# Kernel optimization log

Hardware: AMD Instinct MI355X
Metric: run time of the kernel (lower is better)

Reference implementation:

```python
import jax, jax.numpy as jnp
import numpy as np

# ---- dims ----
B, NP_, NL = 32, 350, 30          # graphs, protein atoms, ligand atoms per graph
NG = NP_ + NL
N = B * NG                        # 12160 nodes
E = B * NP_ * NL                  # 336000 edges (dense bipartite per graph)
HID, HEADS, G = 128, 16, 20
DH = HID // HEADS
KV = 2 * HID + G                  # 276
R_MIN, R_MAX = 0.0, 10.0


def _mlp_params(key, din, dout, hid=HID):
    k1, k2 = jax.random.split(key)
    return (jax.random.normal(k1, (din, hid), jnp.float32) / np.sqrt(din),
            jnp.zeros((hid,), jnp.float32),
            jnp.ones((hid,), jnp.float32),
            jnp.zeros((hid,), jnp.float32),
            jax.random.normal(k2, (hid, dout), jnp.float32) / np.sqrt(hid),
            jnp.zeros((dout,), jnp.float32))


def setup_inputs() -> dict:
    key = jax.random.key(0)
    h = jax.random.normal(jax.random.fold_in(key, 0), (N, HID), jnp.float32)
    x = jax.random.normal(jax.random.fold_in(key, 1), (N, 3), jnp.float32) * 3.0
    # node layout per graph: NP_ protein atoms then NL ligand atoms
    mask_ligand = np.tile(np.concatenate([np.zeros(NP_, np.int64), np.ones(NL, np.int64)]), B)
    base = (np.arange(B) * NG)[:, None]
    prot = base + np.arange(NP_)[None, :]            # [B, NP_]
    lig = base + NP_ + np.arange(NL)[None, :]        # [B, NL]
    # torch: dst = repeat_interleave(protein, NL); src = ligand.repeat(NP_)
    dst = np.repeat(prot, NL, axis=1).reshape(-1)
    src = np.tile(lig, (1, NP_)).reshape(-1)
    inp = {"h": h, "x": x, "src": jnp.asarray(src), "dst": jnp.asarray(dst),
           "mask_ligand": jnp.asarray(mask_ligand)}
    dims = {"hk": (KV, HID), "hv": (KV, HID), "xv": (KV, HEADS), "hq": (HID, HID), "no": (2 * HID, HID)}
    for i, (nm, (di, do)) in enumerate(dims.items()):
        for s, arr in zip(("w1", "b1", "g", "be", "w2", "b2"), _mlp_params(jax.random.fold_in(key, 10 + i), di, do)):
            inp[f"{nm}_{s}"] = arr
    return inp


def _mlp(t, w1, b1, g, be, w2, b2):
    # Linear -> LayerNorm -> ReLU -> Linear
    y = t @ w1 + b1
    mu = y.mean(-1, keepdims=True)
    var = ((y - mu) ** 2).mean(-1, keepdims=True)
    y = jax.nn.relu((y - mu) * jax.lax.rsqrt(var + 1e-5) * g + be)
    return y @ w2 + b2


def _forward(h, x, src, dst, mask_ligand, ps):
    rel_x = x[src] - x[dst]                                   # [E,3]
    dist = jnp.linalg.norm(rel_x, axis=-1, keepdims=True)     # [E,1]
    offset = jnp.linspace(R_MIN, R_MAX, G)
    coeff = -0.5 / (offset[1] - offset[0]) ** 2
    r_feat = jnp.exp(coeff * (dist - offset) ** 2)            # [E,G]; outer_product(v) == v
    # inner layer unpacks (dst_i, src_i) = (src, dst): hi=h[src_i]=h[dst], hj=h[dst_i]=h[src]
    kv = jnp.concatenate([r_feat, h[dst], h[src]], -1)        # [E,KV]
    k = _mlp(kv, *ps["hk"]).reshape(-1, HEADS, DH)            # [E,H,dh]
    q = _mlp(h, *ps["hq"]).reshape(-1, HEADS, DH)             # [N,H,dh]
    logits = (q[src] * k).sum(-1) / np.sqrt(DH)               # [E,H]
    # scatter_softmax over dst_i = src groups (ligand nodes)
    smax = jax.ops.segment_max(logits, src, num_segments=N)
    ex = jnp.exp(logits - smax[src])
    alpha = ex / jax.ops.segment_sum(ex, src, num_segments=N)[src]   # [E,H]
    v = _mlp(kv, *ps["hv"]).reshape(-1, HEADS, DH)            # [E,H,dh]
    xv = _mlp(kv, *ps["xv"])                                  # [E,H]
    m = alpha[:, :, None] * v                                 # [E,H,dh]
    mx = (alpha * xv)[:, :, None] * rel_x[:, None, :]         # [E,H,3]
    out = jax.ops.segment_sum(m, src, num_segments=N).reshape(N, HID)
    out_x = jax.ops.segment_sum(mx, src, num_segments=N)      # [N,H,3]
    # out_fc: h_in[mask_ligand] with int64 mask gathers rows 0/1 (faithful to source)
    out = _mlp(jnp.concatenate([out, h[mask_ligand]], -1), *ps["no"])
    h_out = out + h
    x_out = x + out_x.mean(1)
    return h_out, x_out


def reference(h, x, src, dst, mask_ligand,
              hk_w1, hk_b1, hk_g, hk_be, hk_w2, hk_b2,
              hv_w1, hv_b1, hv_g, hv_be, hv_w2, hv_b2,
              xv_w1, xv_b1, xv_g, xv_be, xv_w2, xv_b2,
              hq_w1, hq_b1, hq_g, hq_be, hq_w2, hq_b2,
              no_w1, no_b1, no_g, no_be, no_w2, no_b2):
    ps = {"hk": (hk_w1, hk_b1, hk_g, hk_be, hk_w2, hk_b2),
          "hv": (hv_w1, hv_b1, hv_g, hv_be, hv_w2, hv_b2),
          "xv": (xv_w1, xv_b1, xv_g, xv_be, xv_w2, xv_b2),
          "hq": (hq_w1, hq_b1, hq_g, hq_be, hq_w2, hq_b2),
          "no": (no_w1, no_b1, no_g, no_be, no_w2, no_b2)}
    return _forward(h, x, src, dst, mask_ligand, ps)
```

## Files before the change

### kernel.cpp

```cpp
#include <hip/hip_runtime.h>
#include <math.h>

namespace {
constexpr int kB = 32;
constexpr int kNP = 350;
constexpr int kNL = 30;
constexpr int kNG = 380;
constexpr int kN = kB * kNG;
constexpr int kG = 20;
constexpr int kNPROT = kB * kNP;
constexpr int kNLIG = kB * kNL;
constexpr int TP = 32;
constexpr int NT = 11;
}

__global__ __launch_bounds__(256) void pre_kernel(
    const float* __restrict__ h,
    const float* __restrict__ wk1, const float* __restrict__ bk1,
    const float* __restrict__ wv1, const float* __restrict__ bv1,
    const float* __restrict__ wx1, const float* __restrict__ bx1,
    float* __restrict__ outKd, float* __restrict__ outVd, float* __restrict__ outXd,
    float* __restrict__ outKs, float* __restrict__ outVs, float* __restrict__ outXs) {
  const int m = blockIdx.y;
  const float* w1 = (m == 0) ? wk1 : (m == 1) ? wv1 : wx1;
  const float* b1 = (m == 0) ? bk1 : (m == 1) ? bv1 : bx1;
  const bool isProt = (blockIdx.x < 175);
  const int rbase = isProt ? blockIdx.x * 64 : (blockIdx.x - 175) * 64;
  float* outArr = isProt ? ((m == 0) ? outKd : (m == 1) ? outVd : outXd)
                         : ((m == 0) ? outKs : (m == 1) ? outVs : outXs);
  const float* wb = w1 + (isProt ? 20 * 128 : 148 * 128);

  __shared__ float sh[64 * 132];
  const int t = threadIdx.x;
#pragma unroll
  for (int j = 0; j < 8; ++j) {
    int flat = t + j * 256;
    int row = flat >> 5;
    int col = (flat & 31) * 4;
    int r = rbase + row;
    int node;
    if (isProt) node = (r / kNP) * kNG + (r % kNP);
    else        node = (r / kNL) * kNG + kNP + (r % kNL);
    *(float4*)&sh[row * 132 + col] = *(const float4*)(h + (size_t)node * 128 + col);
  }
  __syncthreads();

  const int dcol = (t & 31) * 4;
  const int rrow = (t >> 5) * 8;
  float4 acc[8];
#pragma unroll
  for (int i = 0; i < 8; ++i) acc[i] = make_float4(0.f, 0.f, 0.f, 0.f);

  for (int k = 0; k < 128; k += 4) {
    float4 a4[8];
#pragma unroll
    for (int i = 0; i < 8; ++i) a4[i] = *(float4*)&sh[(rrow + i) * 132 + k];
#pragma unroll
    for (int kk = 0; kk < 4; ++kk) {
      float4 w4 = *(const float4*)(wb + (size_t)(k + kk) * 128 + dcol);
#pragma unroll
      for (int i = 0; i < 8; ++i) {
        float a = (kk == 0) ? a4[i].x : (kk == 1) ? a4[i].y : (kk == 2) ? a4[i].z : a4[i].w;
        acc[i].x += a * w4.x; acc[i].y += a * w4.y;
        acc[i].z += a * w4.z; acc[i].w += a * w4.w;
      }
    }
  }
  float4 bias = make_float4(0.f, 0.f, 0.f, 0.f);
  if (!isProt) bias = *(const float4*)(b1 + dcol);
#pragma unroll
  for (int i = 0; i < 8; ++i) {
    float4 o = acc[i];
    o.x += bias.x; o.y += bias.y; o.z += bias.z; o.w += bias.w;
    *(float4*)(outArr + (size_t)(rbase + rrow + i) * 128 + dcol) = o;
  }
}

__global__ __launch_bounds__(128) void cvec_kernel(
    const float* __restrict__ h,
    const float* __restrict__ no_w1, const float* __restrict__ no_b1,
    const float* __restrict__ no_g, const float* __restrict__ no_be,
    const float* __restrict__ no_w2, const float* __restrict__ no_b2,
    float* __restrict__ cvec) {
  __shared__ float sy[128];
  __shared__ float sa[128];
  __shared__ float red[2];
  const int d = threadIdx.x;
  float y = no_b1[d];
  for (int i = 0; i < 128; ++i) y += h[i] * no_w1[(size_t)(128 + i) * 128 + d];
  sy[d] = y;
  __syncthreads();
  if (d == 0) {
    float s = 0.f, ss = 0.f;
    for (int i = 0; i < 128; ++i) { s += sy[i]; ss += sy[i] * sy[i]; }
    float mu = s / 128.f;
    red[0] = mu;
    red[1] = rsqrtf(ss / 128.f - mu * mu + 1e-5f);
  }
  __syncthreads();
  float a = (y - red[0]) * red[1] * no_g[d] + no_be[d];
  sa[d] = fmaxf(a, 0.f);
  __syncthreads();
  float o = no_b2[d];
  for (int i = 0; i < 128; ++i) o += sa[i] * no_w2[(size_t)i * 128 + d];
  cvec[d] = o;
}

__global__ __launch_bounds__(256) void prot_kernel(
    const float* __restrict__ h, const float* __restrict__ x,
    const float* __restrict__ cvec, float* __restrict__ hout, float* __restrict__ xout) {
  int idx = blockIdx.x * 256 + threadIdx.x;
  if (idx < kNPROT * 32) {
    int r = idx >> 5, c4 = (idx & 31) * 4;
    int node = (r / kNP) * kNG + (r % kNP);
    float4 hv = *(const float4*)(h + (size_t)node * 128 + c4);
    float4 cv = *(const float4*)(cvec + c4);
    *(float4*)(hout + (size_t)node * 128 + c4) =
        make_float4(hv.x + cv.x, hv.y + cv.y, hv.z + cv.z, hv.w + cv.w);
  }
  if (idx < kNPROT * 3) {
    int r = idx / 3, c = idx % 3;
    int node = (r / kNP) * kNG + (r % kNP);
    xout[(size_t)node * 3 + c] = x[(size_t)node * 3 + c];
  }
}

struct W20 {
  float4 a0, a1, a2, a3, a4, a5, a6, a7, a8, a9;
  float4 a10, a11, a12, a13, a14, a15, a16, a17, a18, a19;
};

__device__ __forceinline__ W20 load_w20(const float* __restrict__ W, int c4) {
  W20 r;
  r.a0  = *(const float4*)(W + 0 * 128 + c4);
  r.a1  = *(const float4*)(W + 1 * 128 + c4);
  r.a2  = *(const float4*)(W + 2 * 128 + c4);
  r.a3  = *(const float4*)(W + 3 * 128 + c4);
  r.a4  = *(const float4*)(W + 4 * 128 + c4);
  r.a5  = *(const float4*)(W + 5 * 128 + c4);
  r.a6  = *(const float4*)(W + 6 * 128 + c4);
  r.a7  = *(const float4*)(W + 7 * 128 + c4);
  r.a8  = *(const float4*)(W + 8 * 128 + c4);
  r.a9  = *(const float4*)(W + 9 * 128 + c4);
  r.a10 = *(const float4*)(W + 10 * 128 + c4);
  r.a11 = *(const float4*)(W + 11 * 128 + c4);
  r.a12 = *(const float4*)(W + 12 * 128 + c4);
  r.a13 = *(const float4*)(W + 13 * 128 + c4);
  r.a14 = *(const float4*)(W + 14 * 128 + c4);
  r.a15 = *(const float4*)(W + 15 * 128 + c4);
  r.a16 = *(const float4*)(W + 16 * 128 + c4);
  r.a17 = *(const float4*)(W + 17 * 128 + c4);
  r.a18 = *(const float4*)(W + 18 * 128 + c4);
  r.a19 = *(const float4*)(W + 19 * 128 + c4);
  return r;
}

__device__ __forceinline__ float4 gemm20(const W20& w, const float* rfp, float4 yv) {
  const float4 ra = *(const float4*)(rfp + 0);
  const float4 rb = *(const float4*)(rfp + 4);
  const float4 rc = *(const float4*)(rfp + 8);
  const float4 rd = *(const float4*)(rfp + 12);
  const float4 re = *(const float4*)(rfp + 16);
  yv.x += ra.x * w.a0.x;  yv.y += ra.x * w.a0.y;  yv.z += ra.x * w.a0.z;  yv.w += ra.x * w.a0.w;
  yv.x += ra.y * w.a1.x;  yv.y += ra.y * w.a1.y;  yv.z += ra.y * w.a1.z;  yv.w += ra.y * w.a1.w;
  yv.x += ra.z * w.a2.x;  yv.y += ra.z * w.a2.y;  yv.z += ra.z * w.a2.z;  yv.w += ra.z * w.a2.w;
  yv.x += ra.w * w.a3.x;  yv.y += ra.w * w.a3.y;  yv.z += ra.w * w.a3.z;  yv.w += ra.w * w.a3.w;
  yv.x += rb.x * w.a4.x;  yv.y += rb.x * w.a4.y;  yv.z += rb.x * w.a4.z;  yv.w += rb.x * w.a4.w;
  yv.x += rb.y * w.a5.x;  yv.y += rb.y * w.a5.y;  yv.z += rb.y * w.a5.z;  yv.w += rb.y * w.a5.w;
  yv.x += rb.z * w.a6.x;  yv.y += rb.z * w.a6.y;  yv.z += rb.z * w.a6.z;  yv.w += rb.z * w.a6.w;
  yv.x += rb.w * w.a7.x;  yv.y += rb.w * w.a7.y;  yv.z += rb.w * w.a7.z;  yv.w += rb.w * w.a7.w;
  yv.x += rc.x * w.a8.x;  yv.y += rc.x * w.a8.y;  yv.z += rc.x * w.a8.z;  yv.w += rc.x * w.a8.w;
  yv.x += rc.y * w.a9.x;  yv.y += rc.y * w.a9.y;  yv.z += rc.y * w.a9.z;  yv.w += rc.y * w.a9.w;
  yv.x += rc.z * w.a10.x; yv.y += rc.z * w.a10.y; yv.z += rc.z * w.a10.z; yv.w += rc.z * w.a10.w;
  yv.x += rc.w * w.a11.x; yv.y += rc.w * w.a11.y; yv.z += rc.w * w.a11.z; yv.w += rc.w * w.a11.w;
  yv.x += rd.x * w.a12.x; yv.y += rd.x * w.a12.y; yv.z += rd.x * w.a12.z; yv.w += rd.x * w.a12.w;
  yv.x += rd.y * w.a13.x; yv.y += rd.y * w.a13.y; yv.z += rd.y * w.a13.z; yv.w += rd.y * w.a13.w;
  yv.x += rd.z * w.a14.x; yv.y += rd.z * w.a14.y; yv.z += rd.z * w.a14.z; yv.w += rd.z * w.a14.w;
  yv.x += rd.w * w.a15.x; yv.y += rd.w * w.a15.y; yv.z += rd.w * w.a15.z; yv.w += rd.w * w.a15.w;
  yv.x += re.x * w.a16.x; yv.y += re.x * w.a16.y; yv.z += re.x * w.a16.z; yv.w += re.x * w.a16.w;
  yv.x += re.y * w.a17.x; yv.y += re.y * w.a17.y; yv.z += re.y * w.a17.z; yv.w += re.y * w.a17.w;
  yv.x += re.z * w.a18.x; yv.y += re.z * w.a18.y; yv.z += re.z * w.a18.z; yv.w += re.z * w.a18.w;
  yv.x += re.w * w.a19.x; yv.y += re.w * w.a19.y; yv.z += re.w * w.a19.z; yv.w += re.w * w.a19.w;
  return yv;
}

__device__ __forceinline__ void ln_relu_store(float4 yv, float4 g4, float4 be4, float* dst) {
  float s = yv.x + yv.y + yv.z + yv.w;
  float ss = yv.x * yv.x + yv.y * yv.y + yv.z * yv.z + yv.w * yv.w;
  for (int m = 16; m; m >>= 1) { s += __shfl_xor(s, m); ss += __shfl_xor(ss, m); }
  float mu = s * (1.f / 128.f);
  float rs = rsqrtf(ss * (1.f / 128.f) - mu * mu + 1e-5f);
  float4 a;
  a.x = fmaxf((yv.x - mu) * rs * g4.x + be4.x, 0.f);
  a.y = fmaxf((yv.y - mu) * rs * g4.y + be4.y, 0.f);
  a.z = fmaxf((yv.z - mu) * rs * g4.z + be4.z, 0.f);
  a.w = fmaxf((yv.w - mu) * rs * g4.w + be4.w, 0.f);
  *(float4*)dst = a;
}

__device__ __forceinline__ float4 addf4(float4 a, float4 b) {
  return make_float4(a.x + b.x, a.y + b.y, a.z + b.z, a.w + b.w);
}

__global__ __launch_bounds__(256, 2) void edge_kernel(
    const float* __restrict__ h, const float* __restrict__ x,
    const float* __restrict__ preKd, const float* __restrict__ preVd, const float* __restrict__ preXd,
    const float* __restrict__ preKs, const float* __restrict__ preVs, const float* __restrict__ preXs,
    const float* __restrict__ hk_w1, const float* __restrict__ hk_g, const float* __restrict__ hk_be,
    const float* __restrict__ hk_w2, const float* __restrict__ hk_b2,
    const float* __restrict__ hv_w1, const float* __restrict__ hv_g, const float* __restrict__ hv_be,
    const float* __restrict__ hv_w2, const float* __restrict__ hv_b2,
    const float* __restrict__ xv_w1, const float* __restrict__ xv_g, const float* __restrict__ xv_be,
    const float* __restrict__ xv_w2, const float* __restrict__ xv_b2,
    const float* __restrict__ hq_w1, const float* __restrict__ hq_b1, const float* __restrict__ hq_g,
    const float* __restrict__ hq_be, const float* __restrict__ hq_w2, const float* __restrict__ hq_b2,
    const float* __restrict__ no_w1, const float* __restrict__ no_b1, const float* __restrict__ no_g,
    const float* __restrict__ no_be, const float* __restrict__ no_w2, const float* __restrict__ no_b2,
    float* __restrict__ hout, float* __restrict__ xout) {

  __shared__ float smem[13236];
  float* const s_qw    = smem;
  float* const s_logit = smem + 2112;
  float* const s_a     = smem + 7712;
  float* const s_rfu   = smem + 11936;
  float* const s_q     = s_rfu;
  float* const s_outv  = s_rfu + 128;
  float* const s_outx  = s_rfu + 256;
  float* const s_dist  = smem + 12576;
  float* const s_tmp   = smem + 12928;
  float* const s_qb    = smem + 13184;
  float* const s_mx    = smem + 13200;
  float* const s_sum   = smem + 13216;
  float* const s_red   = smem + 13232;

  const int wg = blockIdx.x;
  const int g = wg / kNL, l = wg % kNL;
  const int lignode = g * kNG + kNP + l;
  const int ligidx = g * kNL + l;
  const int t = threadIdx.x;
  const int c4 = (t & 31) * 4;
  const int myp = t >> 5;

  constexpr float kStep = 10.f / 19.f;
  constexpr float kCoeff = -0.5f / (kStep * kStep);

  const float lx0 = x[(size_t)lignode * 3 + 0];
  const float lx1 = x[(size_t)lignode * 3 + 1];
  const float lx2 = x[(size_t)lignode * 3 + 2];

  if (t < 32) *(float4*)&s_tmp[t * 4] = *(const float4*)(h + (size_t)lignode * 128 + t * 4);
  for (int p = t; p < kNP; p += 256) {
    const float* xp = x + (size_t)(g * kNG + p) * 3;
    float r0 = lx0 - xp[0], r1 = lx1 - xp[1], r2 = lx2 - xp[2];
    s_dist[p] = sqrtf(r0 * r0 + r1 * r1 + r2 * r2);
  }
  __syncthreads();

  float yq = 0.f;
  if (t < 128) {
    yq = hq_b1[t];
    for (int k = 0; k < 128; ++k) yq += s_tmp[k] * hq_w1[(size_t)k * 128 + t];
    s_a[t] = yq;
  }
  __syncthreads();
  if (t < 64) {
    float v0 = s_a[t], v1 = s_a[t + 64];
    float s = v0 + v1, ss = v0 * v0 + v1 * v1;
#pragma unroll
    for (int off = 32; off; off >>= 1) { s += __shfl_xor(s, off); ss += __shfl_xor(ss, off); }
    if (t == 0) {
      float mu = s / 128.f;
      s_red[0] = mu;
      s_red[1] = rsqrtf(ss / 128.f - mu * mu + 1e-5f);
    }
  }
  __syncthreads();
  if (t < 128) {
    float a = (yq - s_red[0]) * s_red[1] * hq_g[t] + hq_be[t];
    s_tmp[t] = fmaxf(a, 0.f);
  }
  __syncthreads();
  if (t < 128) {
    float qv = hq_b2[t];
    for (int d = 0; d < 128; ++d) qv += s_tmp[d] * hq_w2[(size_t)d * 128 + t];
    s_q[t] = qv;
  }
  __syncthreads();

  constexpr float kInvSqrtDH = 0.35355339059327379f;
#pragma unroll
  for (int i = 0; i < 8; ++i) {
    int idx = t + i * 256;
    int hh = idx >> 7, d = idx & 127;
    float4 wa = *(const float4*)(hk_w2 + (size_t)d * 128 + hh * 8);
    float4 wb = *(const float4*)(hk_w2 + (size_t)d * 128 + hh * 8 + 4);
    float v = wa.x * s_q[hh * 8 + 0] + wa.y * s_q[hh * 8 + 1] + wa.z * s_q[hh * 8 + 2] +
              wa.w * s_q[hh * 8 + 3] + wb.x * s_q[hh * 8 + 4] + wb.y * s_q[hh * 8 + 5] +
              wb.z * s_q[hh * 8 + 6] + wb.w * s_q[hh * 8 + 7];
    s_qw[hh * 132 + d] = v * kInvSqrtDH;
  }
  if (t < 16) {
    float v = 0.f;
#pragma unroll
    for (int j = 0; j < 8; ++j) v += hk_b2[t * 8 + j] * s_q[t * 8 + j];
    s_qb[t] = v * kInvSqrtDH;
  }
  for (int o = t; o < TP * 20; o += 256) {
    int p = o / 20;
    float dd = s_dist[p] - (o - p * 20) * kStep;
    s_rfu[o] = __expf(kCoeff * dd * dd);
  }
  __syncthreads();

  {
    const W20 w = load_w20(hk_w1, c4);
    const float4 g4 = *(const float4*)(hk_g + c4);
    const float4 be4 = *(const float4*)(hk_be + c4);
    const float4 pres4 = *(const float4*)(preKs + (size_t)ligidx * 128 + c4);

    for (int tile = 0; tile < NT; ++tile) {
      const int p0 = tile * TP;
      const int np = (350 - p0) < TP ? (350 - p0) : TP;
      const int i0 = myp, i1 = myp + 8, i2 = myp + 16, i3 = myp + 24;
      float4 pr0, pr1, pr2, pr3;
      const float* base = preKd + (size_t)(g * kNP + p0) * 128 + c4;
      pr0 = *(const float4*)(base + (size_t)i0 * 128);
      pr1 = *(const float4*)(base + (size_t)i1 * 128);
      pr2 = *(const float4*)(base + (size_t)i2 * 128);
      if (i3 < np) pr3 = *(const float4*)(base + (size_t)i3 * 128);
      ln_relu_store(gemm20(w, &s_rfu[i0 * 20], addf4(pres4, pr0)), g4, be4, &s_a[i0 * 132 + c4]);
      ln_relu_store(gemm20(w, &s_rfu[i1 * 20], addf4(pres4, pr1)), g4, be4, &s_a[i1 * 132 + c4]);
      ln_relu_store(gemm20(w, &s_rfu[i2 * 20], addf4(pres4, pr2)), g4, be4, &s_a[i2 * 132 + c4]);
      if (i3 < np)
        ln_relu_store(gemm20(w, &s_rfu[i3 * 20], addf4(pres4, pr3)), g4, be4, &s_a[i3 * 132 + c4]);
      __syncthreads();
      {
        const int p = t & 31;
        const int h0 = (t >> 5) * 2, h1 = h0 + 1;
        float f0 = 0.f, f1 = 0.f;
#pragma unroll
        for (int d = 0; d < 128; d += 4) {
          float4 a4 = *(float4*)&s_a[p * 132 + d];
          float4 q0 = *(float4*)&s_qw[h0 * 132 + d];
          float4 q1 = *(float4*)&s_qw[h1 * 132 + d];
          f0 += a4.x * q0.x + a4.y * q0.y + a4.z * q0.z + a4.w * q0.w;
          f1 += a4.x * q1.x + a4.y * q1.y + a4.z * q1.z + a4.w * q1.w;
        }
        if (p < np) {
          s_logit[(p0 + p) * 16 + h0] = f0 + s_qb[h0];
          s_logit[(p0 + p) * 16 + h1] = f1 + s_qb[h1];
        }
        const int nxt = (tile + 1 == NT) ? 0 : tile + 1;
        const int q0p = nxt * TP;
        const int nq = (350 - q0p) < TP ? (350 - q0p) : TP;
        for (int o = t; o < nq * 20; o += 256) {
          int pp = o / 20;
          float dd = s_dist[q0p + pp] - (o - pp * 20) * kStep;
          s_rfu[o] = __expf(kCoeff * dd * dd);
        }
      }
      __syncthreads();
    }
  }

  {
    int hh = t & 15, ck = t >> 4;
    float mx = -1e30f;
    for (int p = ck; p < 350; p += 16) mx = fmaxf(mx, s_logit[p * 16 + hh]);
    s_tmp[t] = mx;
  }
  __syncthreads();
  if (t < 16) {
    float mx = s_tmp[t];
    for (int c = 1; c < 16; ++c) mx = fmaxf(mx, s_tmp[c * 16 + t]);
    s_mx[t] = mx;
  }
  __syncthreads();
  {
    int hh = t & 15, ck = t >> 4;
    float mx = s_mx[hh], sm = 0.f;
    for (int p = ck; p < 350; p += 16) sm += __expf(s_logit[p * 16 + hh] - mx);
    s_tmp[t] = sm;
  }
  __syncthreads();
  if (t < 16) {
    float sm = 0.f;
    for (int c = 0; c < 16; ++c) sm += s_tmp[c * 16 + t];
    s_sum[t] = 1.f / sm;
  }
  __syncthreads();
  for (int o = t; o < 350 * 16; o += 256) {
    int hh = o & 15;
    s_logit[o] = __expf(s_logit[o] - s_mx[hh]) * s_sum[hh];
  }
  for (int o = t; o < 2048; o += 256) {
    int hh = o >> 7, d = o & 127;
    s_qw[hh * 132 + d] = xv_w2[(size_t)d * 16 + hh];
  }
  if (t < 16) s_qb[t] = xv_b2[t];
  __syncthreads();

  float accv0 = 0.f, accv1 = 0.f, accv2 = 0.f, accv3 = 0.f;
  float accv4 = 0.f, accv5 = 0.f, accv6 = 0.f, accv7 = 0.f;
  const int dd_ = t & 127;
  const int hb8 = (t >> 7) * 8;
  {
    const W20 w = load_w20(hv_w1, c4);
    const float4 g4 = *(const float4*)(hv_g + c4);
    const float4 be4 = *(const float4*)(hv_be + c4);
    const float4 pres4 = *(const float4*)(preVs + (size_t)ligidx * 128 + c4);

    for (int tile = 0; tile < NT; ++tile) {
      const int p0 = tile * TP;
      const int np = (350 - p0) < TP ? (350 - p0) : TP;
      const int i0 = myp, i1 = myp + 8, i2 = myp + 16, i3 = myp + 24;
      float4 pr0, pr1, pr2, pr3;
      const float* base = preVd + (size_t)(g * kNP + p0) * 128 + c4;
      pr0 = *(const float4*)(base + (size_t)i0 * 128);
      pr1 = *(const float4*)(base + (size_t)i1 * 128);
      pr2 = *(const float4*)(base + (size_t)i2 * 128);
      if (i3 < np) pr3 = *(const float4*)(base + (size_t)i3 * 128);
      ln_relu_store(gemm20(w, &s_rfu[i0 * 20], addf4(pres4, pr0)), g4, be4, &s_a[i0 * 132 + c4]);
      ln_relu_store(gemm20(w, &s_rfu[i1 * 20], addf4(pres4, pr1)), g4, be4, &s_a[i1 * 132 + c4]);
      ln_relu_store(gemm20(w, &s_rfu[i2 * 20], addf4(pres4, pr2)), g4, be4, &s_a[i2 * 132 + c4]);
      if (i3 < np)
        ln_relu_store(gemm20(w, &s_rfu[i3 * 20], addf4(pres4, pr3)), g4, be4, &s_a[i3 * 132 + c4]);
      __syncthreads();
      for (int p = 0; p < np; ++p) {
        float av = s_a[p * 132 + dd_];
        float4 alA = *(float4*)&s_logit[(p0 + p) * 16 + hb8];
        float4 alB = *(float4*)&s_logit[(p0 + p) * 16 + hb8 + 4];
        accv0 += alA.x * av; accv1 += alA.y * av;
        accv2 += alA.z * av; accv3 += alA.w * av;
        accv4 += alB.x * av; accv5 += alB.y * av;
        accv6 += alB.z * av; accv7 += alB.w * av;
      }
      {
        const int nxt = (tile + 1 == NT) ? 0 : tile + 1;
        const int q0p = nxt * TP;
        const int nq = (350 - q0p) < TP ? (350 - q0p) : TP;
        for (int o = t; o < nq * 20; o += 256) {
          int pp = o / 20;
          float dd2 = s_dist[q0p + pp] - (o - pp * 20) * kStep;
          s_rfu[o] = __expf(kCoeff * dd2 * dd2);
        }
      }
      __syncthreads();
    }
  }

  float ax0 = 0.f, ax1 = 0.f, ax2 = 0.f, ax3 = 0.f, ax4 = 0.f, ax5 = 0.f;
  {
    const W20 w = load_w20(xv_w1, c4);
    const float4 g4 = *(const float4*)(xv_g + c4);
    const float4 be4 = *(const float4*)(xv_be + c4);
    const float4 pres4 = *(const float4*)(preXs + (size_t)ligidx * 128 + c4);
    const int p_ = t & 31;
    const int h0 = (t >> 5) * 2, h1 = h0 + 1;

    for (int tile = 0; tile < NT; ++tile) {
      const int p0 = tile * TP;
      const int np = (350 - p0) < TP ? (350 - p0) : TP;
      const int i0 = myp, i1 = myp + 8, i2 = myp + 16, i3 = myp + 24;
      float4 pr0, pr1, pr2, pr3;
      const float* base = preXd + (size_t)(g * kNP + p0) * 128 + c4;
      pr0 = *(const float4*)(base + (size_t)i0 * 128);
      pr1 = *(const float4*)(base + (size_t)i1 * 128);
      pr2 = *(const float4*)(base + (size_t)i2 * 128);
      if (i3 < np) pr3 = *(const float4*)(base + (size_t)i3 * 128);
      ln_relu_store(gemm20(w, &s_rfu[i0 * 20], addf4(pres4, pr0)), g4, be4, &s_a[i0 * 132 + c4]);
      ln_relu_store(gemm20(w, &s_rfu[i1 * 20], addf4(pres4, pr1)), g4, be4, &s_a[i1 * 132 + c4]);
      ln_relu_store(gemm20(w, &s_rfu[i2 * 20], addf4(pres4, pr2)), g4, be4, &s_a[i2 * 132 + c4]);
      if (i3 < np)
        ln_relu_store(gemm20(w, &s_rfu[i3 * 20], addf4(pres4, pr3)), g4, be4, &s_a[i3 * 132 + c4]);
      __syncthreads();
      {
        float f0 = 0.f, f1 = 0.f;
#pragma unroll
        for (int d = 0; d < 128; d += 4) {
          float4 a4 = *(float4*)&s_a[p_ * 132 + d];
          float4 q0 = *(float4*)&s_qw[h0 * 132 + d];
          float4 q1 = *(float4*)&s_qw[h1 * 132 + d];
          f0 += a4.x * q0.x + a4.y * q0.y + a4.z * q0.z + a4.w * q0.w;
          f1 += a4.x * q1.x + a4.y * q1.y + a4.z * q1.z + a4.w * q1.w;
        }
        float w0 = 0.f, w1 = 0.f, r0 = 0.f, r1 = 0.f, r2 = 0.f;
        if (p_ < np) {
          int pg = p0 + p_;
          w0 = s_logit[pg * 16 + h0] * (f0 + s_qb[h0]);
          w1 = s_logit[pg * 16 + h1] * (f1 + s_qb[h1]);
          const float* xp = x + (size_t)(g * kNG + pg) * 3;
          r0 = lx0 - xp[0]; r1 = lx1 - xp[1]; r2 = lx2 - xp[2];
        }
        float p00 = w0 * r0, p01 = w0 * r1, p02 = w0 * r2;
        float p10 = w1 * r0, p11 = w1 * r1, p12 = w1 * r2;
#pragma unroll
        for (int m = 16; m; m >>= 1) {
          p00 += __shfl_xor(p00, m); p01 += __shfl_xor(p01, m); p02 += __shfl_xor(p02, m);
          p10 += __shfl_xor(p10, m); p11 += __shfl_xor(p11, m); p12 += __shfl_xor(p12, m);
        }
        ax0 += p00; ax1 += p01; ax2 += p02;
        ax3 += p10; ax4 += p11; ax5 += p12;
      }
      {
        const int nxt = (tile + 1 == NT) ? 0 : tile + 1;
        const int q0p = nxt * TP;
        const int nq = (350 - q0p) < TP ? (350 - q0p) : TP;
        for (int o = t; o < nq * 20; o += 256) {
          int pp = o / 20;
          float dd2 = s_dist[q0p + pp] - (o - pp * 20) * kStep;
          s_rfu[o] = __expf(kCoeff * dd2 * dd2);
        }
      }
      __syncthreads();
    }
  }

  s_a[(hb8 + 0) * 132 + dd_] = accv0;
  s_a[(hb8 + 1) * 132 + dd_] = accv1;
  s_a[(hb8 + 2) * 132 + dd_] = accv2;
  s_a[(hb8 + 3) * 132 + dd_] = accv3;
  s_a[(hb8 + 4) * 132 + dd_] = accv4;
  s_a[(hb8 + 5) * 132 + dd_] = accv5;
  s_a[(hb8 + 6) * 132 + dd_] = accv6;
  s_a[(hb8 + 7) * 132 + dd_] = accv7;
  {
    const int h0 = (t >> 5) * 2;
    if ((t & 31) == 0) {
      s_outx[h0 * 4 + 0] = ax0; s_outx[h0 * 4 + 1] = ax1; s_outx[h0 * 4 + 2] = ax2;
      s_outx[(h0 + 1) * 4 + 0] = ax3; s_outx[(h0 + 1) * 4 + 1] = ax4;
      s_outx[(h0 + 1) * 4 + 2] = ax5;
    }
  }
  __syncthreads();

  if (t < 128) {
    float o = hv_b2[t];
    const int hh = t >> 3;
    for (int d = 0; d < 128; ++d) o += s_a[hh * 132 + d] * hv_w2[(size_t)d * 128 + t];
    s_outv[t] = o;
  }
  if (t >= 128 && t < 131) {
    int c = t - 128;
    float sm = 0.f;
#pragma unroll
    for (int hh = 0; hh < 16; ++hh) sm += s_outx[hh * 4 + c];
    xout[(size_t)lignode * 3 + c] = x[(size_t)lignode * 3 + c] + sm * (1.f / 16.f);
  }
  __syncthreads();
  float yn = 0.f;
  if (t < 128) {
    yn = no_b1[t];
    for (int i = 0; i < 128; ++i) yn += s_outv[i] * no_w1[(size_t)i * 128 + t];
    const float* h1 = h + 128;
    for (int i = 0; i < 128; ++i) yn += h1[i] * no_w1[(size_t)(128 + i) * 128 + t];
    s_tmp[t] = yn;
  }
  __syncthreads();
  if (t < 64) {
    float v0 = s_tmp[t], v1 = s_tmp[t + 64];
    float s = v0 + v1, ss = v0 * v0 + v1 * v1;
#pragma unroll
    for (int off = 32; off; off >>= 1) { s += __shfl_xor(s, off); ss += __shfl_xor(ss, off); }
    if (t == 0) {
      float mu = s / 128.f;
      s_red[0] = mu;
      s_red[1] = rsqrtf(ss / 128.f - mu * mu + 1e-5f);
    }
  }
  __syncthreads();
  if (t < 128) {
    float a = (yn - s_red[0]) * s_red[1] * no_g[t] + no_be[t];
    s_outv[t] = fmaxf(a, 0.f);
  }
  __syncthreads();
  if (t < 128) {
    float o = no_b2[t];
    for (int d = 0; d < 128; ++d) o += s_outv[d] * no_w2[(size_t)d * 128 + t];
    hout[(size_t)lignode * 128 + t] = o + h[(size_t)lignode * 128 + t];
  }
}

extern "C" void kernel_launch(void* const* d_in, const int* in_sizes, int n_in,
                              void* d_out, int out_size, void* d_ws, size_t ws_size,
                              hipStream_t stream) {
  (void)in_sizes; (void)n_in; (void)out_size; (void)ws_size;
  const float* h = (const float*)d_in[0];
  const float* x = (const float*)d_in[1];
  const float* hk_w1 = (const float*)d_in[5];
  const float* hk_b1 = (const float*)d_in[6];
  const float* hk_g  = (const float*)d_in[7];
  const float* hk_be = (const float*)d_in[8];
  const float* hk_w2 = (const float*)d_in[9];
  const float* hk_b2 = (const float*)d_in[10];
  const float* hv_w1 = (const float*)d_in[11];
  const float* hv_b1 = (const float*)d_in[12];
  const float* hv_g  = (const float*)d_in[13];
  const float* hv_be = (const float*)d_in[14];
  const float* hv_w2 = (const float*)d_in[15];
  const float* hv_b2 = (const float*)d_in[16];
  const float* xv_w1 = (const float*)d_in[17];
  const float* xv_b1 = (const float*)d_in[18];
  const float* xv_g  = (const float*)d_in[19];
  const float* xv_be = (const float*)d_in[20];
  const float* xv_w2 = (const float*)d_in[21];
  const float* xv_b2 = (const float*)d_in[22];
  const float* hq_w1 = (const float*)d_in[23];
  const float* hq_b1 = (const float*)d_in[24];
  const float* hq_g  = (const float*)d_in[25];
  const float* hq_be = (const float*)d_in[26];
  const float* hq_w2 = (const float*)d_in[27];
  const float* hq_b2 = (const float*)d_in[28];
  const float* no_w1 = (const float*)d_in[29];
  const float* no_b1 = (const float*)d_in[30];
  const float* no_g  = (const float*)d_in[31];
  const float* no_be = (const float*)d_in[32];
  const float* no_w2 = (const float*)d_in[33];
  const float* no_b2 = (const float*)d_in[34];

  float* ws = (float*)d_ws;
  float* preKd = ws;
  float* preVd = preKd + (size_t)kNPROT * 128;
  float* preXd = preVd + (size_t)kNPROT * 128;
  float* preKs = preXd + (size_t)kNPROT * 128;
  float* preVs = preKs + (size_t)kNLIG * 128;
  float* preXs = preVs + (size_t)kNLIG * 128;
  float* cvec  = preXs + (size_t)kNLIG * 128;

  float* hout = (float*)d_out;
  float* xout = hout + (size_t)kN * 128;

  pre_kernel<<<dim3(190, 3), dim3(256), 0, stream>>>(
      h, hk_w1, hk_b1, hv_w1, hv_b1, xv_w1, xv_b1,
      preKd, preVd, preXd, preKs, preVs, preXs);
  cvec_kernel<<<dim3(1), dim3(128), 0, stream>>>(
      h, no_w1, no_b1, no_g, no_be, no_w2, no_b2, cvec);
  edge_kernel<<<dim3(960), dim3(256), 0, stream>>>(
      h, x, preKd, preVd, preXd, preKs, preVs, preXs,
      hk_w1, hk_g, hk_be, hk_w2, hk_b2,
      hv_w1, hv_g, hv_be, hv_w2, hv_b2,
      xv_w1, xv_g, xv_be, xv_w2, xv_b2,
      hq_w1, hq_b1, hq_g, hq_be, hq_w2, hq_b2,
      no_w1, no_b1, no_g, no_be, no_w2, no_b2,
      hout, xout);
  prot_kernel<<<dim3(1400), dim3(256), 0, stream>>>(h, x, cvec, hout, xout);
}
```

Before: 694.7 us.

## Restructure edge first-layer GEMM to stream weights and block contiguous rows per thread

The per-thread register-resident 20x4 weight block (W20) is replaced by a loop that loads each weight row from global memory once per tile and applies it to four contiguous protein rows. The RBF features are stored transposed (gaussian-major, padded stride 36) so one float4 shared load feeds four rows. This cuts register pressure, which is why the launch bound drops its minimum-blocks-per-CU hint. The q-weight stride also changes from 132 to 128. The cost is repeated global/L1 weight loads inside the tile loop and possible LDS bank conflicts from the unpadded 128 stride.

```diff
diff --git a/kernel.cpp b/kernel.cpp
--- a/kernel.cpp
+++ b/kernel.cpp
@@ -125,68 +125,10 @@
   }
 }
 
-struct W20 {
-  float4 a0, a1, a2, a3, a4, a5, a6, a7, a8, a9;
-  float4 a10, a11, a12, a13, a14, a15, a16, a17, a18, a19;
-};
-
-__device__ __forceinline__ W20 load_w20(const float* __restrict__ W, int c4) {
-  W20 r;
-  r.a0  = *(const float4*)(W + 0 * 128 + c4);
-  r.a1  = *(const float4*)(W + 1 * 128 + c4);
-  r.a2  = *(const float4*)(W + 2 * 128 + c4);
-  r.a3  = *(const float4*)(W + 3 * 128 + c4);
-  r.a4  = *(const float4*)(W + 4 * 128 + c4);
-  r.a5  = *(const float4*)(W + 5 * 128 + c4);
-  r.a6  = *(const float4*)(W + 6 * 128 + c4);
-  r.a7  = *(const float4*)(W + 7 * 128 + c4);
-  r.a8  = *(const float4*)(W + 8 * 128 + c4);
-  r.a9  = *(const float4*)(W + 9 * 128 + c4);
-  r.a10 = *(const float4*)(W + 10 * 128 + c4);
-  r.a11 = *(const float4*)(W + 11 * 128 + c4);
-  r.a12 = *(const float4*)(W + 12 * 128 + c4);
-  r.a13 = *(const float4*)(W + 13 * 128 + c4);
-  r.a14 = *(const float4*)(W + 14 * 128 + c4);
-  r.a15 = *(const float4*)(W + 15 * 128 + c4);
-  r.a16 = *(const float4*)(W + 16 * 128 + c4);
-  r.a17 = *(const float4*)(W + 17 * 128 + c4);
-  r.a18 = *(const float4*)(W + 18 * 128 + c4);
-  r.a19 = *(const float4*)(W + 19 * 128 + c4);
-  return r;
-}
-
-__device__ __forceinline__ float4 gemm20(const W20& w, const float* rfp, float4 yv) {
-  const float4 ra = *(const float4*)(rfp + 0);
-  const float4 rb = *(const float4*)(rfp + 4);
-  const float4 rc = *(const float4*)(rfp + 8);
-  const float4 rd = *(const float4*)(rfp + 12);
-  const float4 re = *(const float4*)(rfp + 16);
-  yv.x += ra.x * w.a0.x;  yv.y += ra.x * w.a0.y;  yv.z += ra.x * w.a0.z;  yv.w += ra.x * w.a0.w;
-  yv.x += ra.y * w.a1.x;  yv.y += ra.y * w.a1.y;  yv.z += ra.y * w.a1.z;  yv.w += ra.y * w.a1.w;
-  yv.x += ra.z * w.a2.x;  yv.y += ra.z * w.a2.y;  yv.z += ra.z * w.a2.z;  yv.w += ra.z * w.a2.w;
-  yv.x += ra.w * w.a3.x;  yv.y += ra.w * w.a3.y;  yv.z += ra.w * w.a3.z;  yv.w += ra.w * w.a3.w;
-  yv.x += rb.x * w.a4.x;  yv.y += rb.x * w.a4.y;  yv.z += rb.x * w.a4.z;  yv.w += rb.x * w.a4.w;
-  yv.x += rb.y * w.a5.x;  yv.y += rb.y * w.a5.y;  yv.z += rb.y * w.a5.z;  yv.w += rb.y * w.a5.w;
-  yv.x += rb.z * w.a6.x;  yv.y += rb.z * w.a6.y;  yv.z += rb.z * w.a6.z;  yv.w += rb.z * w.a6.w;
-  yv.x += rb.w * w.a7.x;  yv.y += rb.w * w.a7.y;  yv.z += rb.w * w.a7.z;  yv.w += rb.w * w.a7.w;
-  yv.x += rc.x * w.a8.x;  yv.y += rc.x * w.a8.y;  yv.z += rc.x * w.a8.z;  yv.w += rc.x * w.a8.w;
-  yv.x += rc.y * w.a9.x;  yv.y += rc.y * w.a9.y;  yv.z += rc.y * w.a9.z;  yv.w += rc.y * w.a9.w;
-  yv.x += rc.z * w.a10.x; yv.y += rc.z * w.a10.y; yv.z += rc.z * w.a10.z; yv.w += rc.z * w.a10.w;
-  yv.x += rc.w * w.a11.x; yv.y += rc.w * w.a11.y; yv.z += rc.w * w.a11.z; yv.w += rc.w * w.a11.w;
-  yv.x += rd.x * w.a12.x; yv.y += rd.x * w.a12.y; yv.z += rd.x * w.a12.z; yv.w += rd.x * w.a12.w;
-  yv.x += rd.y * w.a13.x; yv.y += rd.y * w.a13.y; yv.z += rd.y * w.a13.z; yv.w += rd.y * w.a13.w;
-  yv.x += rd.z * w.a14.x; yv.y += rd.z * w.a14.y; yv.z += rd.z * w.a14.z; yv.w += rd.z * w.a14.w;
-  yv.x += rd.w * w.a15.x; yv.y += rd.w * w.a15.y; yv.z += rd.w * w.a15.z; yv.w += rd.w * w.a15.w;
-  yv.x += re.x * w.a16.x; yv.y += re.x * w.a16.y; yv.z += re.x * w.a16.z; yv.w += re.x * w.a16.w;
-  yv.x += re.y * w.a17.x; yv.y += re.y * w.a17.y; yv.z += re.y * w.a17.z; yv.w += re.y * w.a17.w;
-  yv.x += re.z * w.a18.x; yv.y += re.z * w.a18.y; yv.z += re.z * w.a18.z; yv.w += re.z * w.a18.w;
-  yv.x += re.w * w.a19.x; yv.y += re.w * w.a19.y; yv.z += re.w * w.a19.z; yv.w += re.w * w.a19.w;
-  return yv;
-}
-
-__device__ __forceinline__ void ln_relu_store(float4 yv, float4 g4, float4 be4, float* dst) {
+__device__ __forceinline__ void ln_row_store(float4 yv, float4 g4, float4 be4, float* dst) {
   float s = yv.x + yv.y + yv.z + yv.w;
   float ss = yv.x * yv.x + yv.y * yv.y + yv.z * yv.z + yv.w * yv.w;
+#pragma unroll
   for (int m = 16; m; m >>= 1) { s += __shfl_xor(s, m); ss += __shfl_xor(ss, m); }
   float mu = s * (1.f / 128.f);
   float rs = rsqrtf(ss * (1.f / 128.f) - mu * mu + 1e-5f);
@@ -198,11 +140,11 @@
   *(float4*)dst = a;
 }
 
-__device__ __forceinline__ float4 addf4(float4 a, float4 b) {
-  return make_float4(a.x + b.x, a.y + b.y, a.z + b.z, a.w + b.w);
-}
-
-__global__ __launch_bounds__(256, 2) void edge_kernel(
+__device__ __forceinline__ void fma4(float4& a, float s, float4 w) {
+  a.x += s * w.x; a.y += s * w.y; a.z += s * w.z; a.w += s * w.w;
+}
+
+__global__ __launch_bounds__(256) void edge_kernel(
     const float* __restrict__ h, const float* __restrict__ x,
     const float* __restrict__ preKd, const float* __restrict__ preVd, const float* __restrict__ preXd,
     const float* __restrict__ preKs, const float* __restrict__ preVs, const float* __restrict__ preXs,
@@ -218,20 +160,20 @@
     const float* __restrict__ no_be, const float* __restrict__ no_w2, const float* __restrict__ no_b2,
     float* __restrict__ hout, float* __restrict__ xout) {
 
-  __shared__ float smem[13236];
+  __shared__ float smem[13250];
   float* const s_qw    = smem;
-  float* const s_logit = smem + 2112;
-  float* const s_a     = smem + 7712;
-  float* const s_rfu   = smem + 11936;
-  float* const s_q     = s_rfu;
-  float* const s_outv  = s_rfu + 128;
-  float* const s_outx  = s_rfu + 256;
-  float* const s_dist  = smem + 12576;
-  float* const s_tmp   = smem + 12928;
-  float* const s_qb    = smem + 13184;
-  float* const s_mx    = smem + 13200;
-  float* const s_sum   = smem + 13216;
-  float* const s_red   = smem + 13232;
+  float* const s_logit = smem + 2048;
+  float* const s_a     = smem + 7648;
+  float* const s_rft   = smem + 11872;
+  float* const s_q     = s_rft;
+  float* const s_outv  = s_rft + 128;
+  float* const s_outx  = s_rft + 256;
+  float* const s_dist  = smem + 12592;
+  float* const s_tmp   = smem + 12944;
+  float* const s_qb    = smem + 13200;
+  float* const s_mx    = smem + 13216;
+  float* const s_sum   = smem + 13232;
+  float* const s_red   = smem + 13248;
 
   const int wg = blockIdx.x;
   const int g = wg / kNL, l = wg % kNL;
@@ -297,7 +239,7 @@
     float v = wa.x * s_q[hh * 8 + 0] + wa.y * s_q[hh * 8 + 1] + wa.z * s_q[hh * 8 + 2] +
               wa.w * s_q[hh * 8 + 3] + wb.x * s_q[hh * 8 + 4] + wb.y * s_q[hh * 8 + 5] +
               wb.z * s_q[hh * 8 + 6] + wb.w * s_q[hh * 8 + 7];
-    s_qw[hh * 132 + d] = v * kInvSqrtDH;
+    s_qw[hh * 128 + d] = v * kInvSqrtDH;
   }
   if (t < 16) {
     float v = 0.f;
@@ -305,15 +247,15 @@
     for (int j = 0; j < 8; ++j) v += hk_b2[t * 8 + j] * s_q[t * 8 + j];
     s_qb[t] = v * kInvSqrtDH;
   }
+  __syncthreads();
   for (int o = t; o < TP * 20; o += 256) {
-    int p = o / 20;
-    float dd = s_dist[p] - (o - p * 20) * kStep;
-    s_rfu[o] = __expf(kCoeff * dd * dd);
+    int p = o & 31, gg = o >> 5;
+    float dd = s_dist[p] - gg * kStep;
+    s_rft[gg * 36 + p] = __expf(kCoeff * dd * dd);
   }
   __syncthreads();
 
   {
-    const W20 w = load_w20(hk_w1, c4);
     const float4 g4 = *(const float4*)(hk_g + c4);
     const float4 be4 = *(const float4*)(hk_be + c4);
     const float4 pres4 = *(const float4*)(preKs + (size_t)ligidx * 128 + c4);
@@ -321,18 +263,28 @@
     for (int tile = 0; tile < NT; ++tile) {
       const int p0 = tile * TP;
       const int np = (350 - p0) < TP ? (350 - p0) : TP;
-      const int i0 = myp, i1 = myp + 8, i2 = myp + 16, i3 = myp + 24;
-      float4 pr0, pr1, pr2, pr3;
+      const int r0 = myp * 4;
       const float* base = preKd + (size_t)(g * kNP + p0) * 128 + c4;
-      pr0 = *(const float4*)(base + (size_t)i0 * 128);
-      pr1 = *(const float4*)(base + (size_t)i1 * 128);
-      pr2 = *(const float4*)(base + (size_t)i2 * 128);
-      if (i3 < np) pr3 = *(const float4*)(base + (size_t)i3 * 128);
-      ln_relu_store(gemm20(w, &s_rfu[i0 * 20], addf4(pres4, pr0)), g4, be4, &s_a[i0 * 132 + c4]);
-      ln_relu_store(gemm20(w, &s_rfu[i1 * 20], addf4(pres4, pr1)), g4, be4, &s_a[i1 * 132 + c4]);
-      ln_relu_store(gemm20(w, &s_rfu[i2 * 20], addf4(pres4, pr2)), g4, be4, &s_a[i2 * 132 + c4]);
-      if (i3 < np)
-        ln_relu_store(gemm20(w, &s_rfu[i3 * 20], addf4(pres4, pr3)), g4, be4, &s_a[i3 * 132 + c4]);
+      float4 a0 = make_float4(0.f, 0.f, 0.f, 0.f), a1 = a0, a2 = a0, a3 = a0;
+      if (r0 + 0 < np) { float4 v = *(const float4*)(base + (size_t)(r0 + 0) * 128);
+        a0 = make_float4(pres4.x + v.x, pres4.y + v.y, pres4.z + v.z, pres4.w + v.w); }
+      if (r0 + 1 < np) { float4 v = *(const float4*)(base + (size_t)(r0 + 1) * 128);
+        a1 = make_float4(pres4.x + v.x, pres4.y + v.y, pres4.z + v.z, pres4.w + v.w); }
+      if (r0 + 2 < np) { float4 v = *(const float4*)(base + (size_t)(r0 + 2) * 128);
+        a2 = make_float4(pres4.x + v.x, pres4.y + v.y, pres4.z + v.z, pres4.w + v.w); }
+      if (r0 + 3 < np) { float4 v = *(const float4*)(base + (size_t)(r0 + 3) * 128);
+        a3 = make_float4(pres4.x + v.x, pres4.y + v.y, pres4.z + v.z, pres4.w + v.w); }
+#pragma unroll 4
+      for (int gg = 0; gg < 20; ++gg) {
+        const float4 w4 = *(const float4*)(hk_w1 + gg * 128 + c4);
+        const float4 rf4 = *(const float4*)&s_rft[gg * 36 + r0];
+        fma4(a0, rf4.x, w4); fma4(a1, rf4.y, w4);
+        fma4(a2, rf4.z, w4); fma4(a3, rf4.w, w4);
+      }
+      if (r0 + 0 < np) ln_row_store(a0, g4, be4, &s_a[(r0 + 0) * 132 + c4]);
+      if (r0 + 1 < np) ln_row_store(a1, g4, be4, &s_a[(r0 + 1) * 132 + c4]);
+      if (r0 + 2 < np) ln_row_store(a2, g4, be4, &s_a[(r0 + 2) * 132 + c4]);
+      if (r0 + 3 < np) ln_row_store(a3, g4, be4, &s_a[(r0 + 3) * 132 + c4]);
       __syncthreads();
       {
         const int p = t & 31;
@@ -341,8 +293,8 @@
 #pragma unroll
         for (int d = 0; d < 128; d += 4) {
           float4 a4 = *(float4*)&s_a[p * 132 + d];
-          float4 q0 = *(float4*)&s_qw[h0 * 132 + d];
-          float4 q1 = *(float4*)&s_qw[h1 * 132 + d];
+          float4 q0 = *(float4*)&s_qw[h0 * 128 + d];
+          float4 q1 = *(float4*)&s_qw[h1 * 128 + d];
           f0 += a4.x * q0.x + a4.y * q0.y + a4.z * q0.z + a4.w * q0.w;
           f1 += a4.x * q1.x + a4.y * q1.y + a4.z * q1.z + a4.w * q1.w;
         }
@@ -353,10 +305,11 @@
         const int nxt = (tile + 1 == NT) ? 0 : tile + 1;
         const int q0p = nxt * TP;
         const int nq = (350 - q0p) < TP ? (350 - q0p) : TP;
-        for (int o = t; o < nq * 20; o += 256) {
-          int pp = o / 20;
-          float dd = s_dist[q0p + pp] - (o - pp * 20) * kStep;
-          s_rfu[o] = __expf(kCoeff * dd * dd);
+        for (int o = t; o < 640; o += 256) {
+          int pp = o & 31, gg = o >> 5;
+          float v = 0.f;
+          if (pp < nq) { float dd = s_dist[q0p + pp] - gg * kStep; v = __expf(kCoeff * dd * dd); }
+          s_rft[gg * 36 + pp] = v;
         }
       }
       __syncthreads();
@@ -395,7 +348,7 @@
   }
   for (int o = t; o < 2048; o += 256) {
     int hh = o >> 7, d = o & 127;
-    s_qw[hh * 132 + d] = xv_w2[(size_t)d * 16 + hh];
+    s_qw[hh * 128 + d] = xv_w2[(size_t)d * 16 + hh];
   }
   if (t < 16) s_qb[t] = xv_b2[t];
   __syncthreads();
@@ -405,7 +358,6 @@
   const int dd_ = t & 127;
   const int hb8 = (t >> 7) * 8;
   {
-    const W20 w = load_w20(hv_w1, c4);
     const float4 g4 = *(const float4*)(hv_g + c4);
     const float4 be4 = *(const float4*)(hv_be + c4);
     const float4 pres4 = *(const float4*)(preVs + (size_t)ligidx * 128 + c4);
@@ -413,18 +365,28 @@
     for (int tile = 0; tile < NT; ++tile) {
       const int p0 = tile * TP;
       const int np = (350 - p0) < TP ? (350 - p0) : TP;
-      const int i0 = myp, i1 = myp + 8, i2 = myp + 16, i3 = myp + 24;
-      float4 pr0, pr1, pr2, pr3;
+      const int r0 = myp * 4;
       const float* base = preVd + (size_t)(g * kNP + p0) * 128 + c4;
-      pr0 = *(const float4*)(base + (size_t)i0 * 128);
-      pr1 = *(const float4*)(base + (size_t)i1 * 128);
-      pr2 = *(const float4*)(base + (size_t)i2 * 128);
-      if (i3 < np) pr3 = *(const float4*)(base + (size_t)i3 * 128);
-      ln_relu_store(gemm20(w, &s_rfu[i0 * 20], addf4(pres4, pr0)), g4, be4, &s_a[i0 * 132 + c4]);
-      ln_relu_store(gemm20(w, &s_rfu[i1 * 20], addf4(pres4, pr1)), g4, be4, &s_a[i1 * 132 + c4]);
-      ln_relu_store(gemm20(w, &s_rfu[i2 * 20], addf4(pres4, pr2)), g4, be4, &s_a[i2 * 132 + c4]);
-      if (i3 < np)
-        ln_relu_store(gemm20(w, &s_rfu[i3 * 20], addf4(pres4, pr3)), g4, be4, &s_a[i3 * 132 + c4]);
+      float4 a0 = make_float4(0.f, 0.f, 0.f, 0.f), a1 = a0, a2 = a0, a3 = a0;
+      if (r0 + 0 < np) { float4 v = *(const float4*)(base + (size_t)(r0 + 0) * 128);
+        a0 = make_float4(pres4.x + v.x, pres4.y + v.y, pres4.z + v.z, pres4.w + v.w); }
+      if (r0 + 1 < np) { float4 v = *(const float4*)(base + (size_t)(r0 + 1) * 128);
+        a1 = make_float4(pres4.x + v.x, pres4.y + v.y, pres4.z + v.z, pres4.w + v.w); }
+      if (r0 + 2 < np) { float4 v = *(const float4*)(base + (size_t)(r0 + 2) * 128);
+        a2 = make_float4(pres4.x + v.x, pres4.y + v.y, pres4.z + v.z, pres4.w + v.w); }
+      if (r0 + 3 < np) { float4 v = *(const float4*)(base + (size_t)(r0 + 3) * 128);
+        a3 = make_float4(pres4.x + v.x, pres4.y + v.y, pres4.z + v.z, pres4.w + v.w); }
+#pragma unroll 4
+      for (int gg = 0; gg < 20; ++gg) {
+        const float4 w4 = *(const float4*)(hv_w1 + gg * 128 + c4);
+        const float4 rf4 = *(const float4*)&s_rft[gg * 36 + r0];
+        fma4(a0, rf4.x, w4); fma4(a1, rf4.y, w4);
+        fma4(a2, rf4.z, w4); fma4(a3, rf4.w, w4);
+      }
+      if (r0 + 0 < np) ln_row_store(a0, g4, be4, &s_a[(r0 + 0) * 132 + c4]);
+      if (r0 + 1 < np) ln_row_store(a1, g4, be4, &s_a[(r0 + 1) * 132 + c4]);
+      if (r0 + 2 < np) ln_row_store(a2, g4, be4, &s_a[(r0 + 2) * 132 + c4]);
+      if (r0 + 3 < np) ln_row_store(a3, g4, be4, &s_a[(r0 + 3) * 132 + c4]);
       __syncthreads();
       for (int p = 0; p < np; ++p) {
         float av = s_a[p * 132 + dd_];
@@ -439,10 +401,11 @@
         const int nxt = (tile + 1 == NT) ? 0 : tile + 1;
         const int q0p = nxt * TP;
         const int nq = (350 - q0p) < TP ? (350 - q0p) : TP;
-        for (int o = t; o < nq * 20; o += 256) {
-          int pp = o / 20;
-          float dd2 = s_dist[q0p + pp] - (o - pp * 20) * kStep;
-          s_rfu[o] = __expf(kCoeff * dd2 * dd2);
+        for (int o = t; o < 640; o += 256) {
+          int pp = o & 31, gg = o >> 5;
+          float v = 0.f;
+          if (pp < nq) { float dd = s_dist[q0p + pp] - gg * kStep; v = __expf(kCoeff * dd * dd); }
+          s_rft[gg * 36 + pp] = v;
         }
       }
       __syncthreads();
@@ -451,7 +414,6 @@
 
   float ax0 = 0.f, ax1 = 0.f, ax2 = 0.f, ax3 = 0.f, ax4 = 0.f, ax5 = 0.f;
   {
-    const W20 w = load_w20(xv_w1, c4);
     const float4 g4 = *(const float4*)(xv_g + c4);
     const float4 be4 = *(const float4*)(xv_be + c4);
     const float4 pres4 = *(const float4*)(preXs + (size_t)ligidx * 128 + c4);
@@ -461,39 +423,49 @@
     for (int tile = 0; tile < NT; ++tile) {
       const int p0 = tile * TP;
       const int np = (350 - p0) < TP ? (350 - p0) : TP;
-      const int i0 = myp, i1 = myp + 8, i2 = myp + 16, i3 = myp + 24;
-      float4 pr0, pr1, pr2, pr3;
+      const int r0 = myp * 4;
       const float* base = preXd + (size_t)(g * kNP + p0) * 128 + c4;
-      pr0 = *(const float4*)(base + (size_t)i0 * 128);
-      pr1 = *(const float4*)(base + (size_t)i1 * 128);
-      pr2 = *(const float4*)(base + (size_t)i2 * 128);
-      if (i3 < np) pr3 = *(const float4*)(base + (size_t)i3 * 128);
-      ln_relu_store(gemm20(w, &s_rfu[i0 * 20], addf4(pres4, pr0)), g4, be4, &s_a[i0 * 132 + c4]);
-      ln_relu_store(gemm20(w, &s_rfu[i1 * 20], addf4(pres4, pr1)), g4, be4, &s_a[i1 * 132 + c4]);
-      ln_relu_store(gemm20(w, &s_rfu[i2 * 20], addf4(pres4, pr2)), g4, be4, &s_a[i2 * 132 + c4]);
-      if (i3 < np)
-        ln_relu_store(gemm20(w, &s_rfu[i3 * 20], addf4(pres4, pr3)), g4, be4, &s_a[i3 * 132 + c4]);
+      float4 a0 = make_float4(0.f, 0.f, 0.f, 0.f), a1 = a0, a2 = a0, a3 = a0;
+      if (r0 + 0 < np) { float4 v = *(const float4*)(base + (size_t)(r0 + 0) * 128);
+        a0 = make_float4(pres4.x + v.x, pres4.y + v.y, pres4.z + v.z, pres4.w + v.w); }
+      if (r0 + 1 < np) { float4 v = *(const float4*)(base + (size_t)(r0 + 1) * 128);
+        a1 = make_float4(pres4.x + v.x, pres4.y + v.y, pres4.z + v.z, pres4.w + v.w); }
+      if (r0 + 2 < np) { float4 v = *(const float4*)(base + (size_t)(r0 + 2) * 128);
+        a2 = make_float4(pres4.x + v.x, pres4.y + v.y, pres4.z + v.z, pres4.w + v.w); }
+      if (r0 + 3 < np) { float4 v = *(const float4*)(base + (size_t)(r0 + 3) * 128);
+        a3 = make_float4(pres4.x + v.x, pres4.y + v.y, pres4.z + v.z, pres4.w + v.w); }
+#pragma unroll 4
+      for (int gg = 0; gg < 20; ++gg) {
+        const float4 w4 = *(const float4*)(xv_w1 + gg * 128 + c4);
+        const float4 rf4 = *(const float4*)&s_rft[gg * 36 + r0];
+        fma4(a0, rf4.x, w4); fma4(a1, rf4.y, w4);
+        fma4(a2, rf4.z, w4); fma4(a3, rf4.w, w4);
+      }
+      if (r0 + 0 < np) ln_row_store(a0, g4, be4, &s_a[(r0 + 0) * 132 + c4]);
+      if (r0 + 1 < np) ln_row_store(a1, g4, be4, &s_a[(r0 + 1) * 132 + c4]);
+      if (r0 + 2 < np) ln_row_store(a2, g4, be4, &s_a[(r0 + 2) * 132 + c4]);
+      if (r0 + 3 < np) ln_row_store(a3, g4, be4, &s_a[(r0 + 3) * 132 + c4]);
       __syncthreads();
       {
         float f0 = 0.f, f1 = 0.f;
 #pragma unroll
         for (int d = 0; d < 128; d += 4) {
           float4 a4 = *(float4*)&s_a[p_ * 132 + d];
-          float4 q0 = *(float4*)&s_qw[h0 * 132 + d];
-          float4 q1 = *(float4*)&s_qw[h1 * 132 + d];
+          float4 q0 = *(float4*)&s_qw[h0 * 128 + d];
+          float4 q1 = *(float4*)&s_qw[h1 * 128 + d];
           f0 += a4.x * q0.x + a4.y * q0.y + a4.z * q0.z + a4.w * q0.w;
           f1 += a4.x * q1.x + a4.y * q1.y + a4.z * q1.z + a4.w * q1.w;
         }
-        float w0 = 0.f, w1 = 0.f, r0 = 0.f, r1 = 0.f, r2 = 0.f;
+        float w0 = 0.f, w1 = 0.f, r0x = 0.f, r1x = 0.f, r2x = 0.f;
         if (p_ < np) {
           int pg = p0 + p_;
           w0 = s_logit[pg * 16 + h0] * (f0 + s_qb[h0]);
           w1 = s_logit[pg * 16 + h1] * (f1 + s_qb[h1]);
           const float* xp = x + (size_t)(g * kNG + pg) * 3;
-          r0 = lx0 - xp[0]; r1 = lx1 - xp[1]; r2 = lx2 - xp[2];
-        }
-        float p00 = w0 * r0, p01 = w0 * r1, p02 = w0 * r2;
-        float p10 = w1 * r0, p11 = w1 * r1, p12 = w1 * r2;
+          r0x = lx0 - xp[0]; r1x = lx1 - xp[1]; r2x = lx2 - xp[2];
+        }
+        float p00 = w0 * r0x, p01 = w0 * r1x, p02 = w0 * r2x;
+        float p10 = w1 * r0x, p11 = w1 * r1x, p12 = w1 * r2x;
 #pragma unroll
         for (int m = 16; m; m >>= 1) {
           p00 += __shfl_xor(p00, m); p01 += __shfl_xor(p01, m); p02 += __shfl_xor(p02, m);
@@ -506,10 +478,11 @@
         const int nxt = (tile + 1 == NT) ? 0 : tile + 1;
         const int q0p = nxt * TP;
         const int nq = (350 - q0p) < TP ? (350 - q0p) : TP;
-        for (int o = t; o < nq * 20; o += 256) {
-          int pp = o / 20;
-          float dd2 = s_dist[q0p + pp] - (o - pp * 20) * kStep;
-          s_rfu[o] = __expf(kCoeff * dd2 * dd2);
+        for (int o = t; o < 640; o += 256) {
+          int pp = o & 31, gg = o >> 5;
+          float v = 0.f;
+          if (pp < nq) { float dd = s_dist[q0p + pp] - gg * kStep; v = __expf(kCoeff * dd * dd); }
+          s_rft[gg * 36 + pp] = v;
         }
       }
       __syncthreads();
```

Result: slower. 952.1 us (+37.1%).
